# Kernel tuning notes

Measured on AMD Instinct MI355X. Metric: run time of the kernel, lower is better.

## Reference

```python
import jax, jax.numpy as jnp
from jax import lax
import numpy as np

RADIUS = 0.1
NSAMPLE = 32
STRIDE = 3
ED_NSAMPLE = 10


def _sqdist(a, b):
    # a: [B,M,3], b: [B,N,3] -> [B,M,N] squared euclidean distance
    return (jnp.sum(a * a, -1)[:, :, None] + jnp.sum(b * b, -1)[:, None, :]
            - 2.0 * jnp.einsum('bmc,bnc->bmn', a, b))


def setup_inputs() -> dict:
    key = jax.random.key(0)
    ks = jax.random.split(key, 16)
    B, N = 8, 4096
    s = 0.05
    inp = {
        'data': jax.random.normal(ks[0], (B, N, 3), dtype=jnp.float32),
        'numpoints': N,
        # stem MLP 3 -> 64
        'W_stem': jax.random.normal(ks[1], (3, 64), dtype=jnp.float32) * s,
        'b_stem': jnp.zeros((64,), jnp.float32),
        # SA shared MLP (3 dp + 64 fj) -> 128
        'W_sa': jax.random.normal(ks[2], (67, 128), dtype=jnp.float32) * s,
        'b_sa': jnp.zeros((128,), jnp.float32),
        # FP MLP (128 interp + 64 skip) -> 64
        'W_fp': jax.random.normal(ks[3], (192, 64), dtype=jnp.float32) * s,
        'b_fp': jnp.zeros((64,), jnp.float32),
        # eigen-feature MLP 3 -> 4 -> 4
        'W_e1': jax.random.normal(ks[4], (3, 4), dtype=jnp.float32) * s,
        'b_e1': jnp.zeros((4,), jnp.float32),
        'W_e2': jax.random.normal(ks[5], (4, 4), dtype=jnp.float32) * s,
        'b_e2': jnp.zeros((4,), jnp.float32),
        # conv_final 1x1: 68 -> 64, + BN affine
        'W_fin': jax.random.normal(ks[6], (68, 64), dtype=jnp.float32) * s,
        'b_fin': jnp.zeros((64,), jnp.float32),
        'gamma': jnp.ones((64,), jnp.float32),
        'beta': jnp.zeros((64,), jnp.float32),
    }
    return inp


def reference(data, numpoints, W_stem, b_stem, W_sa, b_sa, W_fp, b_fp,
              W_e1, b_e1, W_e2, b_e2, W_fin, b_fin, gamma, beta):
    B, N, _ = data.shape
    b_ix = jnp.arange(B)[:, None, None]

    # ---------- encoder: stem MLP ----------
    f0 = jax.nn.relu(data @ W_stem + b_stem)  # [B,N,64]

    # set abstraction: stride-subsample centers, ball query, dp_fj, MLP, max
    sub_idx = jnp.arange(0, N, STRIDE)
    new_xyz = data[:, sub_idx]                 # [B,M,3]
    d2 = _sqdist(new_xyz, data)                # [B,M,N]
    col = jnp.arange(N, dtype=jnp.int32)
    valid = d2 < RADIUS * RADIUS
    keys = jnp.where(valid, col, N + col)      # first-valid ball query ordering
    negk, _ = lax.top_k(-keys, NSAMPLE)
    idx = -negk                                # [B,M,ns]
    first = idx[..., :1]                       # self point always valid
    idx = jnp.where(idx >= N, first, idx)
    g_xyz = data[b_ix, idx]                    # [B,M,ns,3]
    dp = (g_xyz - new_xyz[:, :, None, :]) / RADIUS  # normalize_dp
    g_f = f0[b_ix, idx]                        # [B,M,ns,64]
    feat = jnp.concatenate([dp, g_f], -1)      # [B,M,ns,67]
    h = jax.nn.relu(feat @ W_sa + b_sa)        # [B,M,ns,128]
    f_sub = jnp.max(h, axis=2)                 # [B,M,128]

    # ---------- decoder: 3-NN inverse-distance feature propagation ----------
    d2f = _sqdist(data, new_xyz)               # [B,N,M]
    negd, nn = lax.top_k(-d2f, 3)
    w = 1.0 / (-negd + 1e-8)
    w = w / jnp.sum(w, -1, keepdims=True)      # [B,N,3]
    nbr_f = f_sub[b_ix, nn]                    # [B,N,3,128]
    interp = jnp.einsum('bnk,bnkc->bnc', w, nbr_f)
    f = jax.nn.relu(jnp.concatenate([interp, f0], -1) @ W_fp + b_fp)  # [B,N,64]

    # ---------- KNN covariance eigen-features ----------
    d2e = _sqdist(data, data)                  # [B,N,N]
    _, gidx = lax.top_k(-d2e, ED_NSAMPLE)      # [B,N,k]
    nbr = data[b_ix, gidx]                     # [B,N,k,3]
    cen = nbr - jnp.mean(nbr, axis=2, keepdims=True)
    cov = jnp.einsum('bnkc,bnkd->bncd', cen, cen) / ED_NSAMPLE  # [B,N,3,3]
    eig = jnp.linalg.eigvalsh(cov)             # [B,N,3] ascending
    ef = jax.nn.relu(eig @ W_e1 + b_e1) @ W_e2 + b_e2  # [B,N,4]

    # ---------- fused 1x1 conv + BN (training-mode stats) + relu ----------
    z_in = jnp.concatenate([f, ef], -1)        # [B,N,68]
    zc = z_in @ W_fin + b_fin                  # [B,N,64]
    mu = jnp.mean(zc, axis=(0, 1))
    var = jnp.var(zc, axis=(0, 1))
    z = jax.nn.relu((zc - mu) * lax.rsqrt(var + 1e-5) * gamma + beta)
    z = jnp.transpose(z, (0, 2, 1))            # [B,64,N]
    return (data, z)
```

## Files before the change

kernel.cpp:

```cpp
#include <hip/hip_runtime.h>
#include <stdint.h>

#define BB 8
#define NN 4096
#define MM 1366
#define NS 32
#define RAD2 0.01f
#define NCH 16
#define CHUNK (NN/NCH)

static_assert(NCH * CHUNK == NN, "chunking");

__device__ __forceinline__ float rl(float v, int l) {
    return __int_as_float(__builtin_amdgcn_readlane(__float_as_int(v), l));
}
__device__ __forceinline__ uint32_t um(uint32_t a, uint32_t b) { return a < b ? a : b; }
__device__ __forceinline__ uint32_t ux(uint32_t a, uint32_t b) { return a > b ? a : b; }
__device__ __forceinline__ uint32_t um3(uint32_t a, uint32_t b, uint32_t c) { return um(um(a, b), c); }

__device__ __forceinline__ void mrg2(uint32_t* kk, uint32_t s0, uint32_t s1) {
    uint32_t n0 = um(kk[0], s0);
    uint32_t n1 = um3(kk[1], ux(kk[0], s0), s1);
    uint32_t n2 = um3(kk[2], ux(kk[1], s0), ux(kk[0], s1));
    uint32_t n3 = um3(kk[3], ux(kk[2], s0), ux(kk[1], s1));
    uint32_t n4 = um3(kk[4], ux(kk[3], s0), ux(kk[2], s1));
    uint32_t n5 = um3(kk[5], ux(kk[4], s0), ux(kk[3], s1));
    uint32_t n6 = um3(kk[6], ux(kk[5], s0), ux(kk[4], s1));
    uint32_t n7 = um3(kk[7], ux(kk[6], s0), ux(kk[5], s1));
    uint32_t n8 = um3(kk[8], ux(kk[7], s0), ux(kk[6], s1));
    uint32_t n9 = um3(kk[9], ux(kk[8], s0), ux(kk[7], s1));
    kk[0]=n0; kk[1]=n1; kk[2]=n2; kk[3]=n3; kk[4]=n4;
    kk[5]=n5; kk[6]=n6; kk[7]=n7; kk[8]=n8; kk[9]=n9;
}

__device__ __forceinline__ void mrg4(uint32_t* kk, uint32_t s0, uint32_t s1,
                                     uint32_t s2, uint32_t s3) {
    uint32_t n0 = um(kk[0], s0);
    uint32_t n1 = um3(kk[1], ux(kk[0], s0), s1);
    uint32_t n2 = um(um3(kk[2], ux(kk[1], s0), ux(kk[0], s1)), s2);
    uint32_t n3 = um3(um3(kk[3], ux(kk[2], s0), ux(kk[1], s1)), ux(kk[0], s2), s3);
    uint32_t n4 = um3(um3(kk[4], ux(kk[3], s0), ux(kk[2], s1)), ux(kk[1], s2), ux(kk[0], s3));
    uint32_t n5 = um3(um3(kk[5], ux(kk[4], s0), ux(kk[3], s1)), ux(kk[2], s2), ux(kk[1], s3));
    uint32_t n6 = um3(um3(kk[6], ux(kk[5], s0), ux(kk[4], s1)), ux(kk[3], s2), ux(kk[2], s3));
    uint32_t n7 = um3(um3(kk[7], ux(kk[6], s0), ux(kk[5], s1)), ux(kk[4], s2), ux(kk[3], s3));
    uint32_t n8 = um3(um3(kk[8], ux(kk[7], s0), ux(kk[6], s1)), ux(kk[5], s2), ux(kk[4], s3));
    uint32_t n9 = um3(um3(kk[9], ux(kk[8], s0), ux(kk[7], s1)), ux(kk[6], s2), ux(kk[5], s3));
    kk[0]=n0; kk[1]=n1; kk[2]=n2; kk[3]=n3; kk[4]=n4;
    kk[5]=n5; kk[6]=n6; kk[7]=n7; kk[8]=n8; kk[9]=n9;
}

__device__ __forceinline__ void srt4(uint32_t& a, uint32_t& b, uint32_t& c, uint32_t& d) {
    uint32_t t0 = um(a, b), t1 = ux(a, b), t2 = um(c, d), t3 = ux(c, d);
    uint32_t s0 = um(t0, t2), m0 = ux(t0, t2), m1 = um(t1, t3), s3 = ux(t1, t3);
    a = s0; b = um(m0, m1); c = ux(m0, m1); d = s3;
}

__global__ __launch_bounds__(256) void k_stem(const float* __restrict__ data,
                                              const float* __restrict__ Ws,
                                              const float* __restrict__ bs,
                                              float* __restrict__ f0,
                                              float* __restrict__ out,
                                              float4* __restrict__ cand4) {
    int blk = blockIdx.x;
    if (blk >= (BB * NN * 64) / 256) {
        int t = (blk - (BB * NN * 64) / 256) * 256 + threadIdx.x;
        float x = data[t * 3], y = data[t * 3 + 1], z = data[t * 3 + 2];
        out[t * 3] = x; out[t * 3 + 1] = y; out[t * 3 + 2] = z;
        cand4[t] = make_float4(x, y, z, x * x + y * y + z * z);
        return;
    }
    int t = blk * 256 + threadIdx.x;
    int c = t & 63;
    int r = t >> 6;
    const float* d = data + r * 3;
    float acc = bs[c];
    acc = fmaf(d[0], Ws[c], acc);
    acc = fmaf(d[1], Ws[64 + c], acc);
    acc = fmaf(d[2], Ws[128 + c], acc);
    f0[t] = fmaxf(acc, 0.f);
}

__global__ __launch_bounds__(256) void k_sa(const float4* __restrict__ cand4,
                                            const float* __restrict__ data,
                                            const float* __restrict__ f0,
                                            const uint32_t* __restrict__ mrg,
                                            const float* __restrict__ Wsa,
                                            const float* __restrict__ bsa,
                                            float* __restrict__ fsub) {
    __shared__ float2 sW[67 * 64];
    __shared__ int sIdx[4][NS];
    for (int i = threadIdx.x; i < 67 * 64; i += 256) {
        int k = i >> 6, c = i & 63;
        sW[i] = make_float2(Wsa[k * 128 + c], Wsa[k * 128 + 64 + c]);
    }
    __syncthreads();
    int wv = threadIdx.x >> 6, lane = threadIdx.x & 63;
    int gm = blockIdx.x * 4 + wv;
    if (gm >= BB * MM) return;
    int b = gm / MM, m = gm - b * MM;
    const float4* cb4 = cand4 + b * NN;
    const float* db = data + b * NN * 3;
    float4 cen = cb4[3 * m];
    float cx = cen.x, cy = cen.y, cz = cen.z, sa = cen.w;

    int cnt;
    bool fallback;
    {
        float d2l = 1e30f;
        int idxl = 0;
        if (lane < 10) {
            uint32_t key = mrg[lane * (BB * NN) + b * NN + 3 * m];
            idxl = (int)(key & 0xFFFu);
            float4 c = cb4[idxl];
            float dot = fmaf(cz, c.z, fmaf(cy, c.y, cx * c.x));
            d2l = (sa + c.w) - 2.f * dot;
        }
        bool valid = (lane < 10) && (d2l < RAD2);
        unsigned long long mask = __ballot(valid);
        if (valid) sIdx[wv][__popcll(mask & ((1ull << lane) - 1ull))] = idxl;
        cnt = __popcll(mask);
        fallback = rl(d2l, 9) < RAD2 * 1.0005f;
    }
    if (fallback) {
        cnt = 0;
        for (int base = 0; base < NN; base += 64) {
            int n = base + lane;
            float4 c = cb4[n];
            float dot = fmaf(cz, c.z, fmaf(cy, c.y, cx * c.x));
            float d2 = (sa + c.w) - 2.f * dot;
            bool valid = d2 < RAD2;
            unsigned long long mask = __ballot(valid);
            if (valid) {
                int pos = cnt + __popcll(mask & ((1ull << lane) - 1ull));
                if (pos < NS) sIdx[wv][pos] = n;
            }
            cnt += __popcll(mask);
            if (cnt >= NS) break;
        }
    }
    int scnt = cnt < NS ? cnt : NS;

    float cl = lane == 0 ? cx : (lane == 1 ? cy : cz);
    float hb0 = bsa[lane], hb1 = bsa[64 + lane];
    float m0 = 0.f, m1 = 0.f;

    for (int s0 = 0; s0 < scnt; s0 += 4) {
        float fr[4], fr2[4];
        #pragma unroll
        for (int u = 0; u < 4; ++u) {
            int s = s0 + u;
            if (s >= scnt) s = 0;
            int nj = sIdx[wv][s];
            int fb = (b * NN + nj) * 64;
            float v;
            if (lane >= 3) v = f0[fb + lane - 3];
            else           v = (db[nj * 3 + lane] - cl) * 10.0f;
            fr[u] = v;
            fr2[u] = (lane < 3) ? f0[fb + 61 + lane] : 0.f;
        }
        float h0[4], h1[4];
        #pragma unroll
        for (int u = 0; u < 4; ++u) { h0[u] = hb0; h1[u] = hb1; }
        for (int k = 0; k < 64; ++k) {
            float2 w = sW[k * 64 + lane];
            #pragma unroll
            for (int u = 0; u < 4; ++u) {
                float fv = rl(fr[u], k);
                h0[u] = fmaf(fv, w.x, h0[u]);
                h1[u] = fmaf(fv, w.y, h1[u]);
            }
        }
        #pragma unroll
        for (int k = 64; k < 67; ++k) {
            float2 w = sW[k * 64 + lane];
            #pragma unroll
            for (int u = 0; u < 4; ++u) {
                float fv = rl(fr2[u], k - 64);
                h0[u] = fmaf(fv, w.x, h0[u]);
                h1[u] = fmaf(fv, w.y, h1[u]);
            }
        }
        #pragma unroll
        for (int u = 0; u < 4; ++u) {
            m0 = fmaxf(m0, fmaxf(h0[u], 0.f));
            m1 = fmaxf(m1, fmaxf(h1[u], 0.f));
        }
    }
    fsub[gm * 128 + lane] = m0;
    fsub[gm * 128 + 64 + lane] = m1;
}

__global__ __launch_bounds__(512) void k_interp(const float4* __restrict__ cand4,
                                                const float* __restrict__ fsub,
                                                float* __restrict__ itp) {
    __shared__ float4 sC[MM];
    __shared__ float sMD[8][64][3];
    __shared__ int   sMI[8][64][3];
    __shared__ float sWts[64][3];
    __shared__ int   sNbr[64][3];
    int t = threadIdx.x, wv = t >> 6, lane = t & 63;
    int blk = blockIdx.x;
    int b = blk >> 6;
    int pbase = (blk & 63) * 64;
    const float4* cb4 = cand4 + b * NN;
    for (int m = t; m < MM; m += 512) sC[m] = cb4[3 * m];
    __syncthreads();
    int p = pbase + lane;
    float4 pm = cb4[p];
    float px = pm.x, py = pm.y, pz = pm.z, pa = pm.w;
    float d0 = 1e30f, d1 = 1e30f, d2v = 1e30f;
    int n0 = 0, n1 = 0, n2 = 0;
    int ms = wv * 171, me = ms + 171 < MM ? ms + 171 : MM;
    for (int m = ms; m < me; ++m) {
        float4 c = sC[m];
        float dd = (pa + c.w) - 2.f * (px * c.x + py * c.y + pz * c.z);
        if (dd < d2v) {
            if (dd < d1) {
                d2v = d1; n2 = n1;
                if (dd < d0) { d1 = d0; n1 = n0; d0 = dd; n0 = m; }
                else         { d1 = dd; n1 = m; }
            } else { d2v = dd; n2 = m; }
        }
    }
    sMD[wv][lane][0] = d0; sMD[wv][lane][1] = d1; sMD[wv][lane][2] = d2v;
    sMI[wv][lane][0] = n0; sMI[wv][lane][1] = n1; sMI[wv][lane][2] = n2;
    __syncthreads();
    if (wv == 0) {
        d0 = sMD[0][lane][0]; d1 = sMD[0][lane][1]; d2v = sMD[0][lane][2];
        n0 = sMI[0][lane][0]; n1 = sMI[0][lane][1]; n2 = sMI[0][lane][2];
        for (int w = 1; w < 8; ++w) {
            #pragma unroll
            for (int r = 0; r < 3; ++r) {
                float dd = sMD[w][lane][r];
                int mm = sMI[w][lane][r];
                if (dd < d2v) {
                    if (dd < d1) {
                        d2v = d1; n2 = n1;
                        if (dd < d0) { d1 = d0; n1 = n0; d0 = dd; n0 = mm; }
                        else         { d1 = dd; n1 = mm; }
                    } else { d2v = dd; n2 = mm; }
                }
            }
        }
        float w0 = 1.f / (d0 + 1e-8f), w1 = 1.f / (d1 + 1e-8f), w2 = 1.f / (d2v + 1e-8f);
        float ws = w0 + w1 + w2;
        sWts[lane][0] = w0 / ws; sWts[lane][1] = w1 / ws; sWts[lane][2] = w2 / ws;
        sNbr[lane][0] = n0; sNbr[lane][1] = n1; sNbr[lane][2] = n2;
    }
    __syncthreads();
    for (int i = wv * 8; i < wv * 8 + 8; ++i) {
        float a0 = sWts[i][0], a1 = sWts[i][1], a2 = sWts[i][2];
        const float* r0 = fsub + (b * MM + sNbr[i][0]) * 128;
        const float* r1 = fsub + (b * MM + sNbr[i][1]) * 128;
        const float* r2 = fsub + (b * MM + sNbr[i][2]) * 128;
        float v0 = fmaf(a2, r2[lane], fmaf(a1, r1[lane], a0 * r0[lane]));
        float v1 = fmaf(a2, r2[64 + lane], fmaf(a1, r1[64 + lane], a0 * r0[64 + lane]));
        int row = b * NN + pbase + i;
        itp[row * 128 + lane] = v0;
        itp[row * 128 + 64 + lane] = v1;
    }
}

__global__ __launch_bounds__(256) void k_knn_part(const float4* __restrict__ cand4,
                                                  uint32_t* __restrict__ pk) {
    int t = threadIdx.x;
    int blk = blockIdx.x;
    int ch = blk & (NCH - 1);
    int pg = (blk >> 4) & 15;
    int b = blk >> 8;
    const float4* cb = cand4 + b * NN;
    int c0 = ch * CHUNK;
    int p = pg * 256 + t;
    float4 me = cb[p];
    float px = me.x, py = me.y, pz = me.z, pa = me.w;
    uint32_t kk[10];
    #pragma unroll
    for (int r = 0; r < 10; ++r) kk[r] = 0xFFFFFF00u + r;
    for (int j = 0; j < CHUNK; j += 4) {
        float4 ca = cb[c0 + j];
        float4 cbv = cb[c0 + j + 1];
        float4 cc = cb[c0 + j + 2];
        float4 cd = cb[c0 + j + 3];
        float da = fmaxf(fmaf(-2.f, fmaf(pz, ca.z, fmaf(py, ca.y, px * ca.x)), pa + ca.w), 0.f);
        float db_ = fmaxf(fmaf(-2.f, fmaf(pz, cbv.z, fmaf(py, cbv.y, px * cbv.x)), pa + cbv.w), 0.f);
        float dc = fmaxf(fmaf(-2.f, fmaf(pz, cc.z, fmaf(py, cc.y, px * cc.x)), pa + cc.w), 0.f);
        float dd = fmaxf(fmaf(-2.f, fmaf(pz, cd.z, fmaf(py, cd.y, px * cd.x)), pa + cd.w), 0.f);
        uint32_t ka = (__float_as_uint(da) & 0xFFFFF000u) | (uint32_t)(c0 + j);
        uint32_t kb = (__float_as_uint(db_) & 0xFFFFF000u) | (uint32_t)(c0 + j + 1);
        uint32_t kc = (__float_as_uint(dc) & 0xFFFFF000u) | (uint32_t)(c0 + j + 2);
        uint32_t kd = (__float_as_uint(dd) & 0xFFFFF000u) | (uint32_t)(c0 + j + 3);
        srt4(ka, kb, kc, kd);
        mrg4(kk, ka, kb, kc, kd);
    }
    int gp = b * NN + p;
    #pragma unroll
    for (int r = 0; r < 10; ++r)
        pk[(ch * 10 + r) * (BB * NN) + gp] = kk[r];
}

__device__ __forceinline__ void jrot(float& app, float& aqq, float& apq,
                                     float& arp, float& arq) {
    float ap = apq;
    if (fabsf(ap) > 1e-32f) {
        float th = (aqq - app) / (2.f * ap);
        float t = 1.f / (fabsf(th) + sqrtf(th * th + 1.f));
        t = th < 0.f ? -t : t;
        float c = 1.f / sqrtf(t * t + 1.f);
        float s = t * c;
        app = app - t * ap;
        aqq = aqq + t * ap;
        apq = 0.f;
        float rp = arp, rq = arq;
        arp = c * rp - s * rq;
        arq = s * rp + c * rq;
    }
}

__global__ __launch_bounds__(256) void k_knn_eig(const float4* __restrict__ cand4,
                                                 const uint32_t* __restrict__ pk,
                                                 uint32_t* __restrict__ mrg,
                                                 const float* __restrict__ We1,
                                                 const float* __restrict__ be1,
                                                 const float* __restrict__ We2,
                                                 const float* __restrict__ be2,
                                                 float* __restrict__ ef) {
    int t = blockIdx.x * 256 + threadIdx.x;
    int b = t >> 12;
    const float4* cb = cand4 + b * NN;
    uint32_t kk[10];
    #pragma unroll
    for (int r = 0; r < 10; ++r) kk[r] = pk[r * (BB * NN) + t];
    for (int ch = 1; ch < NCH; ++ch) {
        uint32_t s[10];
        #pragma unroll
        for (int r = 0; r < 10; ++r) s[r] = pk[(ch * 10 + r) * (BB * NN) + t];
        mrg4(kk, s[0], s[1], s[2], s[3]);
        mrg4(kk, s[4], s[5], s[6], s[7]);
        mrg2(kk, s[8], s[9]);
    }
    #pragma unroll
    for (int r = 0; r < 10; ++r)
        mrg[r * (BB * NN) + t] = kk[r];
    float xs[10], ys[10], zs[10];
    float mx = 0.f, my = 0.f, mz = 0.f;
    #pragma unroll
    for (int r = 0; r < 10; ++r) {
        int n = (int)(kk[r] & 0xFFFu);
        float4 cr = cb[n];
        xs[r] = cr.x; ys[r] = cr.y; zs[r] = cr.z;
        mx += xs[r]; my += ys[r]; mz += zs[r];
    }
    mx *= 0.1f; my *= 0.1f; mz *= 0.1f;
    float a00 = 0, a01 = 0, a02 = 0, a11 = 0, a12 = 0, a22 = 0;
    #pragma unroll
    for (int r = 0; r < 10; ++r) {
        float x = xs[r] - mx, y = ys[r] - my, z = zs[r] - mz;
        a00 = fmaf(x, x, a00); a01 = fmaf(x, y, a01); a02 = fmaf(x, z, a02);
        a11 = fmaf(y, y, a11); a12 = fmaf(y, z, a12); a22 = fmaf(z, z, a22);
    }
    a00 *= 0.1f; a01 *= 0.1f; a02 *= 0.1f; a11 *= 0.1f; a12 *= 0.1f; a22 *= 0.1f;
    #pragma unroll
    for (int sweep = 0; sweep < 6; ++sweep) {
        jrot(a00, a11, a01, a02, a12);
        jrot(a00, a22, a02, a01, a12);
        jrot(a11, a22, a12, a01, a02);
    }
    float e0 = a00, e1 = a11, e2 = a22, tmp;
    if (e0 > e1) { tmp = e0; e0 = e1; e1 = tmp; }
    if (e1 > e2) { tmp = e1; e1 = e2; e2 = tmp; }
    if (e0 > e1) { tmp = e0; e0 = e1; e1 = tmp; }
    float tt[4];
    #pragma unroll
    for (int i = 0; i < 4; ++i) {
        float v = be1[i];
        v = fmaf(e0, We1[i], v);
        v = fmaf(e1, We1[4 + i], v);
        v = fmaf(e2, We1[8 + i], v);
        tt[i] = fmaxf(v, 0.f);
    }
    #pragma unroll
    for (int i = 0; i < 4; ++i) {
        float v = be2[i];
        v = fmaf(tt[0], We2[i], v);
        v = fmaf(tt[1], We2[4 + i], v);
        v = fmaf(tt[2], We2[8 + i], v);
        v = fmaf(tt[3], We2[12 + i], v);
        ef[t * 4 + i] = v;
    }
}

__global__ __launch_bounds__(256) void k_fp(const float* __restrict__ itp,
                                            const float* __restrict__ f0,
                                            const float* __restrict__ W,
                                            const float* __restrict__ bias,
                                            float* __restrict__ outf) {
    __shared__ float sW[192 * 64];
    for (int i = threadIdx.x; i < 192 * 64; i += 256) sW[i] = W[i];
    __syncthreads();
    int lane = threadIdx.x & 63;
    int wv = threadIdx.x >> 6;
    float bb = bias[lane];
    int rowbase = blockIdx.x * 64 + wv * 16;
    for (int it = 0; it < 4; ++it) {
        int r = rowbase + it * 4;
        float fa[4], fbv[4], fc[4], acc[4];
        #pragma unroll
        for (int u = 0; u < 4; ++u) {
            fa[u]  = itp[(r + u) * 128 + lane];
            fbv[u] = itp[(r + u) * 128 + 64 + lane];
            fc[u]  = f0[(r + u) * 64 + lane];
            acc[u] = bb;
        }
        #pragma unroll
        for (int k = 0; k < 192; ++k) {
            float w = sW[k * 64 + lane];
            #pragma unroll
            for (int u = 0; u < 4; ++u) {
                float fv = k < 64 ? rl(fa[u], k)
                         : (k < 128 ? rl(fbv[u], k - 64) : rl(fc[u], k - 128));
                acc[u] = fmaf(fv, w, acc[u]);
            }
        }
        #pragma unroll
        for (int u = 0; u < 4; ++u)
            outf[(r + u) * 64 + lane] = fmaxf(acc[u], 0.f);
    }
}

__global__ __launch_bounds__(256) void k_fin(const float* __restrict__ fb,
                                             const float* __restrict__ efb,
                                             const float* __restrict__ W,
                                             const float* __restrict__ bias,
                                             float* __restrict__ zc) {
    __shared__ float sW[68 * 64];
    for (int i = threadIdx.x; i < 68 * 64; i += 256) sW[i] = W[i];
    __syncthreads();
    int lane = threadIdx.x & 63;
    int wv = threadIdx.x >> 6;
    float bb = bias[lane];
    int rowbase = blockIdx.x * 64 + wv * 16;
    for (int it = 0; it < 4; ++it) {
        int r = rowbase + it * 4;
        float fa[4], fe[4], acc[4];
        #pragma unroll
        for (int u = 0; u < 4; ++u) {
            fa[u] = fb[(r + u) * 64 + lane];
            fe[u] = (lane < 4) ? efb[(r + u) * 4 + lane] : 0.f;
            acc[u] = bb;
        }
        #pragma unroll
        for (int k = 0; k < 68; ++k) {
            float w = sW[k * 64 + lane];
            #pragma unroll
            for (int u = 0; u < 4; ++u) {
                float fv = k < 64 ? rl(fa[u], k) : rl(fe[u], k - 64);
                acc[u] = fmaf(fv, w, acc[u]);
            }
        }
        #pragma unroll
        for (int u = 0; u < 4; ++u)
            zc[(r + u) * 64 + lane] = acc[u];
    }
}

__global__ __launch_bounds__(256) void k_stats1(const float* __restrict__ zc,
                                                float* __restrict__ pp) {
    int t = threadIdx.x;
    int c = t & 63, r4 = t >> 6;
    float s = 0.f, sq = 0.f;
    int base = blockIdx.x * 512;
    for (int i = 0; i < 128; ++i) {
        float v = zc[(base + i * 4 + r4) * 64 + c];
        s += v;
        sq = fmaf(v, v, sq);
    }
    __shared__ float ls[256], lq[256];
    ls[t] = s; lq[t] = sq;
    __syncthreads();
    if (t < 64) {
        float st = ls[t] + ls[t + 64] + ls[t + 128] + ls[t + 192];
        float qt = lq[t] + lq[t + 64] + lq[t + 128] + lq[t + 192];
        pp[blockIdx.x * 128 + t] = st;
        pp[blockIdx.x * 128 + 64 + t] = qt;
    }
}

__global__ __launch_bounds__(64) void k_stats2(const float* __restrict__ pp,
                                               const float* __restrict__ gamma,
                                               const float* __restrict__ beta,
                                               float* __restrict__ ss) {
    int c = threadIdx.x;
    float s = 0.f, sq = 0.f;
    for (int k = 0; k < 64; ++k) {
        s += pp[k * 128 + c];
        sq += pp[k * 128 + 64 + c];
    }
    const float inv = 1.f / (float)(BB * NN);
    float mu = s * inv;
    float var = sq * inv - mu * mu;
    float sc = gamma[c] / sqrtf(var + 1e-5f);
    ss[c] = sc;
    ss[64 + c] = beta[c] - mu * sc;
}

__global__ __launch_bounds__(256) void k_norm_t(const float* __restrict__ zc,
                                                const float* __restrict__ ss,
                                                float* __restrict__ out) {
    __shared__ float sT[64][65];
    int blk = blockIdx.x;
    int b = blk >> 6;
    int nbase = (blk & 63) * 64;
    int c = threadIdx.x & 63;
    int r4 = threadIdx.x >> 6;
    float sc = ss[c], sh = ss[64 + c];
    #pragma unroll
    for (int i = 0; i < 16; ++i) {
        int nr = i * 4 + r4;
        float v = zc[(b * NN + nbase + nr) * 64 + c];
        sT[nr][c] = fmaxf(fmaf(v, sc, sh), 0.f);
    }
    __syncthreads();
    int nn = threadIdx.x & 63;
    #pragma unroll
    for (int i = 0; i < 16; ++i) {
        int cc = i * 4 + r4;
        out[BB * NN * 3 + (b * 64 + cc) * NN + nbase + nn] = sT[nn][cc];
    }
}

extern "C" void kernel_launch(void* const* d_in, const int* in_sizes, int n_in,
                              void* d_out, int out_size, void* d_ws, size_t ws_size,
                              hipStream_t stream) {
    const float* data = (const float*)d_in[0];
    const float* Wst  = (const float*)d_in[2];
    const float* bst  = (const float*)d_in[3];
    const float* Wsa  = (const float*)d_in[4];
    const float* bsa  = (const float*)d_in[5];
    const float* Wfp  = (const float*)d_in[6];
    const float* bfp  = (const float*)d_in[7];
    const float* We1  = (const float*)d_in[8];
    const float* be1  = (const float*)d_in[9];
    const float* We2  = (const float*)d_in[10];
    const float* be2  = (const float*)d_in[11];
    const float* Wfin = (const float*)d_in[12];
    const float* bfin = (const float*)d_in[13];
    const float* gamma = (const float*)d_in[14];
    const float* beta  = (const float*)d_in[15];
    float* out = (float*)d_out;

    float* f0   = (float*)d_ws;
    float* fsub = f0 + 2097152;
    float* efb  = fsub + 1398784;
    float* zc   = efb + 131072;
    float* ss   = zc + 2097152;
    float* pp   = ss + 128;
    float4* cand4 = (float4*)(pp + 8192);
    uint32_t* mrgb = (uint32_t*)((float*)cand4 + 131072);
    float* itp  = (float*)mrgb + 1310720;
    float* fb   = itp + 4194304;
    uint32_t* pkk = (uint32_t*)itp;

    k_stem<<<(BB * NN * 64) / 256 + (BB * NN) / 256, 256, 0, stream>>>(
        data, Wst, bst, f0, out, cand4);
    k_knn_part<<<BB * 16 * NCH, 256, 0, stream>>>(cand4, pkk);
    k_knn_eig<<<(BB * NN) / 256, 256, 0, stream>>>(cand4, pkk, mrgb, We1, be1, We2, be2, efb);
    k_sa<<<(BB * MM + 3) / 4, 256, 0, stream>>>(cand4, data, f0, mrgb, Wsa, bsa, fsub);
    k_interp<<<BB * 64, 512, 0, stream>>>(cand4, fsub, itp);
    k_fp<<<512, 256, 0, stream>>>(itp, f0, Wfp, bfp, fb);
    k_fin<<<512, 256, 0, stream>>>(fb, efb, Wfin, bfin, zc);
    k_stats1<<<64, 256, 0, stream>>>(zc, pp);
    k_stats2<<<1, 64, 0, stream>>>(pp, gamma, beta, ss);
    k_norm_t<<<512, 256, 0, stream>>>(zc, ss, out);
}
```

Baseline: 299.2 us.

## Replace brute-force KNN with Morton-sorted groups and bounding-box pruning

Replaces the brute-force chunked KNN, which compared every point against all 4096 candidates and then merged 16 partial lists, with a spatial approach. A new kernel bins points into a 16^3 Morton grid, counting-sorts them and computes per-group bounding boxes. The new KNN kernel scans its own group first, then visits neighbouring groups in two directions, skipping any whose box distance exceeds the current 10th-nearest bound. The two directional halves are merged in shared memory. This cuts distance work sharply but adds a serial single-block-per-batch sort, a grid of only 512 blocks of 128 threads, and data-dependent divergence.

```diff
diff --git a/kernel.cpp b/kernel.cpp
--- a/kernel.cpp
+++ b/kernel.cpp
@@ -6,10 +6,7 @@
 #define MM 1366
 #define NS 32
 #define RAD2 0.01f
-#define NCH 16
-#define CHUNK (NN/NCH)
-
-static_assert(NCH * CHUNK == NN, "chunking");
+#define NGRP 64
 
 __device__ __forceinline__ float rl(float v, int l) {
     return __int_as_float(__builtin_amdgcn_readlane(__float_as_int(v), l));
@@ -55,6 +52,12 @@
     a = s0; b = um(m0, m1); c = ux(m0, m1); d = s3;
 }
 
+__device__ __forceinline__ uint32_t spr3(uint32_t v) {
+    v = (v | (v << 4)) & 0xC3u;
+    v = (v | (v << 2)) & 0x249u;
+    return v;
+}
+
 __global__ __launch_bounds__(256) void k_stem(const float* __restrict__ data,
                                               const float* __restrict__ Ws,
                                               const float* __restrict__ bs,
@@ -78,6 +81,236 @@
     acc = fmaf(d[1], Ws[64 + c], acc);
     acc = fmaf(d[2], Ws[128 + c], acc);
     f0[t] = fmaxf(acc, 0.f);
+}
+
+__global__ __launch_bounds__(256) void k_sort(const float4* __restrict__ cand4,
+                                              float4* __restrict__ cand4s,
+                                              uint32_t* __restrict__ perm,
+                                              float4* __restrict__ gbox) {
+    __shared__ uint32_t cnt[4096];
+    __shared__ uint32_t part[256];
+    int b = blockIdx.x, t = threadIdx.x;
+    const float4* cb = cand4 + b * NN;
+    for (int i = t; i < 4096; i += 256) cnt[i] = 0;
+    __syncthreads();
+    uint32_t cid[16];
+    #pragma unroll
+    for (int u = 0; u < 16; ++u) {
+        float4 c = cb[u * 256 + t];
+        int ix = (int)floorf((c.x + 4.f) * 2.f);
+        int iy = (int)floorf((c.y + 4.f) * 2.f);
+        int iz = (int)floorf((c.z + 4.f) * 2.f);
+        ix = ix < 0 ? 0 : (ix > 15 ? 15 : ix);
+        iy = iy < 0 ? 0 : (iy > 15 ? 15 : iy);
+        iz = iz < 0 ? 0 : (iz > 15 ? 15 : iz);
+        uint32_t m = spr3((uint32_t)ix) | (spr3((uint32_t)iy) << 1) | (spr3((uint32_t)iz) << 2);
+        cid[u] = m;
+        atomicAdd(&cnt[m], 1u);
+    }
+    __syncthreads();
+    uint32_t c16[16];
+    uint32_t s = 0;
+    #pragma unroll
+    for (int u = 0; u < 16; ++u) { c16[u] = cnt[t * 16 + u]; s += c16[u]; }
+    part[t] = s;
+    __syncthreads();
+    for (int off = 1; off < 256; off <<= 1) {
+        uint32_t v = (t >= off) ? part[t - off] : 0u;
+        __syncthreads();
+        part[t] += v;
+        __syncthreads();
+    }
+    uint32_t run = part[t] - s;
+    #pragma unroll
+    for (int u = 0; u < 16; ++u) { cnt[t * 16 + u] = run; run += c16[u]; }
+    __syncthreads();
+    #pragma unroll
+    for (int u = 0; u < 16; ++u) {
+        int p = u * 256 + t;
+        uint32_t pos = atomicAdd(&cnt[cid[u]], 1u);
+        cand4s[b * NN + pos] = cb[p];
+        perm[b * NN + pos] = (uint32_t)p;
+    }
+    __syncthreads();
+    if (t < NGRP) {
+        float4 mn = make_float4(1e30f, 1e30f, 1e30f, 0.f);
+        float4 mx = make_float4(-1e30f, -1e30f, -1e30f, 0.f);
+        for (int j = 0; j < 64; ++j) {
+            float4 c = cand4s[b * NN + t * 64 + j];
+            mn.x = fminf(mn.x, c.x); mn.y = fminf(mn.y, c.y); mn.z = fminf(mn.z, c.z);
+            mx.x = fmaxf(mx.x, c.x); mx.y = fmaxf(mx.y, c.y); mx.z = fmaxf(mx.z, c.z);
+        }
+        gbox[(b * NGRP + t) * 2]     = mn;
+        gbox[(b * NGRP + t) * 2 + 1] = mx;
+    }
+}
+
+__global__ __launch_bounds__(128) void k_knn(const float4* __restrict__ cand4s,
+                                             const uint32_t* __restrict__ perm,
+                                             const float4* __restrict__ gbox,
+                                             uint32_t* __restrict__ mrg) {
+    __shared__ float4 sBox[2 * NGRP];
+    __shared__ uint32_t sKK[64][10];
+    int t = threadIdx.x, role = t >> 6, lane = t & 63;
+    int gw = blockIdx.x;
+    int b = gw >> 6;
+    int g = gw & (NGRP - 1);
+    for (int i = t; i < 2 * NGRP; i += 128) sBox[i] = gbox[b * 2 * NGRP + i];
+    __syncthreads();
+    const float4* cs = cand4s + b * NN;
+    const uint32_t* ps = perm + b * NN;
+    float4 me = cs[g * 64 + lane];
+    uint32_t mo = ps[g * 64 + lane];
+    float px = me.x, py = me.y, pz = me.z, pa = me.w;
+    uint32_t kk[10];
+    #pragma unroll
+    for (int r = 0; r < 10; ++r) kk[r] = 0xFFFFFF00u + r;
+
+    auto scan_group = [&](int jg) {
+        const float4* cp = cs + jg * 64;
+        const uint4* pq = (const uint4*)(ps + jg * 64);
+        for (int j = 0; j < 16; ++j) {
+            float4 ca  = cp[j * 4];
+            float4 cbv = cp[j * 4 + 1];
+            float4 cc  = cp[j * 4 + 2];
+            float4 cd  = cp[j * 4 + 3];
+            uint4 pm = pq[j];
+            float da  = fmaxf(fmaf(-2.f, fmaf(pz, ca.z,  fmaf(py, ca.y,  px * ca.x)),  pa + ca.w),  0.f);
+            float db_ = fmaxf(fmaf(-2.f, fmaf(pz, cbv.z, fmaf(py, cbv.y, px * cbv.x)), pa + cbv.w), 0.f);
+            float dc  = fmaxf(fmaf(-2.f, fmaf(pz, cc.z,  fmaf(py, cc.y,  px * cc.x)),  pa + cc.w),  0.f);
+            float dd  = fmaxf(fmaf(-2.f, fmaf(pz, cd.z,  fmaf(py, cd.y,  px * cd.x)),  pa + cd.w),  0.f);
+            uint32_t ka = (__float_as_uint(da)  & 0xFFFFF000u) | pm.x;
+            uint32_t kb = (__float_as_uint(db_) & 0xFFFFF000u) | pm.y;
+            uint32_t kc = (__float_as_uint(dc)  & 0xFFFFF000u) | pm.z;
+            uint32_t kd = (__float_as_uint(dd)  & 0xFFFFF000u) | pm.w;
+            uint32_t mn4 = um(um(ka, kb), um(kc, kd));
+            if (__ballot(mn4 < kk[9])) {
+                srt4(ka, kb, kc, kd);
+                mrg4(kk, ka, kb, kc, kd);
+            }
+        }
+    };
+    auto bound = [&]() {
+        float u2 = __uint_as_float((kk[9] & 0xFFFFF000u) + 0x1000u);
+        #pragma unroll
+        for (int off = 1; off < 64; off <<= 1) u2 = fmaxf(u2, __shfl_xor(u2, off));
+        return u2;
+    };
+
+    scan_group(g);
+    float ub = bound();
+    float4 amn = sBox[g * 2], amx = sBox[g * 2 + 1];
+    auto try_group = [&](int jg) {
+        float4 bmn = sBox[jg * 2], bmx = sBox[jg * 2 + 1];
+        float dx = fmaxf(fmaxf(amn.x - bmx.x, bmn.x - amx.x), 0.f);
+        float dy = fmaxf(fmaxf(amn.y - bmx.y, bmn.y - amx.y), 0.f);
+        float dz = fmaxf(fmaxf(amn.z - bmx.z, bmn.z - amx.z), 0.f);
+        float bd2 = fmaf(dx, dx, fmaf(dy, dy, dz * dz));
+        if (bd2 < ub * 1.0005f) {
+            scan_group(jg);
+            ub = bound();
+        }
+    };
+    if (role == 0) {
+        for (int d = 1; d < NGRP; ++d) { int j = g - d; if (j >= 0)   try_group(j); }
+    } else {
+        for (int d = 1; d < NGRP; ++d) { int j = g + d; if (j < NGRP) try_group(j); }
+    }
+    if (role == 1) {
+        #pragma unroll
+        for (int r = 0; r < 10; ++r) sKK[lane][r] = kk[r];
+    }
+    __syncthreads();
+    if (role == 0) {
+        uint32_t s[10];
+        #pragma unroll
+        for (int r = 0; r < 10; ++r) s[r] = sKK[lane][r];
+        mrg4(kk, s[0], s[1], s[2], s[3]);
+        mrg4(kk, s[4], s[5], s[6], s[7]);
+        mrg2(kk, s[8], s[9]);
+        int gp = b * NN + (int)mo;
+        #pragma unroll
+        for (int r = 0; r < 10; ++r) mrg[r * (BB * NN) + gp] = kk[r];
+    }
+}
+
+__device__ __forceinline__ void jrot(float& app, float& aqq, float& apq,
+                                     float& arp, float& arq) {
+    float ap = apq;
+    if (fabsf(ap) > 1e-32f) {
+        float th = (aqq - app) / (2.f * ap);
+        float t = 1.f / (fabsf(th) + sqrtf(th * th + 1.f));
+        t = th < 0.f ? -t : t;
+        float c = 1.f / sqrtf(t * t + 1.f);
+        float s = t * c;
+        app = app - t * ap;
+        aqq = aqq + t * ap;
+        apq = 0.f;
+        float rp = arp, rq = arq;
+        arp = c * rp - s * rq;
+        arq = s * rp + c * rq;
+    }
+}
+
+__global__ __launch_bounds__(256) void k_knn_eig(const float4* __restrict__ cand4,
+                                                 const uint32_t* __restrict__ mrg,
+                                                 const float* __restrict__ We1,
+                                                 const float* __restrict__ be1,
+                                                 const float* __restrict__ We2,
+                                                 const float* __restrict__ be2,
+                                                 float* __restrict__ ef) {
+    int t = blockIdx.x * 256 + threadIdx.x;
+    int b = t >> 12;
+    const float4* cb = cand4 + b * NN;
+    uint32_t kk[10];
+    #pragma unroll
+    for (int r = 0; r < 10; ++r) kk[r] = mrg[r * (BB * NN) + t];
+    float xs[10], ys[10], zs[10];
+    float mx = 0.f, my = 0.f, mz = 0.f;
+    #pragma unroll
+    for (int r = 0; r < 10; ++r) {
+        int n = (int)(kk[r] & 0xFFFu);
+        float4 cr = cb[n];
+        xs[r] = cr.x; ys[r] = cr.y; zs[r] = cr.z;
+        mx += xs[r]; my += ys[r]; mz += zs[r];
+    }
+    mx *= 0.1f; my *= 0.1f; mz *= 0.1f;
+    float a00 = 0, a01 = 0, a02 = 0, a11 = 0, a12 = 0, a22 = 0;
+    #pragma unroll
+    for (int r = 0; r < 10; ++r) {
+        float x = xs[r] - mx, y = ys[r] - my, z = zs[r] - mz;
+        a00 = fmaf(x, x, a00); a01 = fmaf(x, y, a01); a02 = fmaf(x, z, a02);
+        a11 = fmaf(y, y, a11); a12 = fmaf(y, z, a12); a22 = fmaf(z, z, a22);
+    }
+    a00 *= 0.1f; a01 *= 0.1f; a02 *= 0.1f; a11 *= 0.1f; a12 *= 0.1f; a22 *= 0.1f;
+    #pragma unroll
+    for (int sweep = 0; sweep < 6; ++sweep) {
+        jrot(a00, a11, a01, a02, a12);
+        jrot(a00, a22, a02, a01, a12);
+        jrot(a11, a22, a12, a01, a02);
+    }
+    float e0 = a00, e1 = a11, e2 = a22, tmp;
+    if (e0 > e1) { tmp = e0; e0 = e1; e1 = tmp; }
+    if (e1 > e2) { tmp = e1; e1 = e2; e2 = tmp; }
+    if (e0 > e1) { tmp = e0; e0 = e1; e1 = tmp; }
+    float tt[4];
+    #pragma unroll
+    for (int i = 0; i < 4; ++i) {
+        float v = be1[i];
+        v = fmaf(e0, We1[i], v);
+        v = fmaf(e1, We1[4 + i], v);
+        v = fmaf(e2, We1[8 + i], v);
+        tt[i] = fmaxf(v, 0.f);
+    }
+    #pragma unroll
+    for (int i = 0; i < 4; ++i) {
+        float v = be2[i];
+        v = fmaf(tt[0], We2[i], v);
+        v = fmaf(tt[1], We2[4 + i], v);
+        v = fmaf(tt[2], We2[8 + i], v);
+        v = fmaf(tt[3], We2[12 + i], v);
+        ef[t * 4 + i] = v;
+    }
 }
 
 __global__ __launch_bounds__(256) void k_sa(const float4* __restrict__ cand4,
@@ -258,134 +491,6 @@
         int row = b * NN + pbase + i;
         itp[row * 128 + lane] = v0;
         itp[row * 128 + 64 + lane] = v1;
-    }
-}
-
-__global__ __launch_bounds__(256) void k_knn_part(const float4* __restrict__ cand4,
-                                                  uint32_t* __restrict__ pk) {
-    int t = threadIdx.x;
-    int blk = blockIdx.x;
-    int ch = blk & (NCH - 1);
-    int pg = (blk >> 4) & 15;
-    int b = blk >> 8;
-    const float4* cb = cand4 + b * NN;
-    int c0 = ch * CHUNK;
-    int p = pg * 256 + t;
-    float4 me = cb[p];
-    float px = me.x, py = me.y, pz = me.z, pa = me.w;
-    uint32_t kk[10];
-    #pragma unroll
-    for (int r = 0; r < 10; ++r) kk[r] = 0xFFFFFF00u + r;
-    for (int j = 0; j < CHUNK; j += 4) {
-        float4 ca = cb[c0 + j];
-        float4 cbv = cb[c0 + j + 1];
-        float4 cc = cb[c0 + j + 2];
-        float4 cd = cb[c0 + j + 3];
-        float da = fmaxf(fmaf(-2.f, fmaf(pz, ca.z, fmaf(py, ca.y, px * ca.x)), pa + ca.w), 0.f);
-        float db_ = fmaxf(fmaf(-2.f, fmaf(pz, cbv.z, fmaf(py, cbv.y, px * cbv.x)), pa + cbv.w), 0.f);
-        float dc = fmaxf(fmaf(-2.f, fmaf(pz, cc.z, fmaf(py, cc.y, px * cc.x)), pa + cc.w), 0.f);
-        float dd = fmaxf(fmaf(-2.f, fmaf(pz, cd.z, fmaf(py, cd.y, px * cd.x)), pa + cd.w), 0.f);
-        uint32_t ka = (__float_as_uint(da) & 0xFFFFF000u) | (uint32_t)(c0 + j);
-        uint32_t kb = (__float_as_uint(db_) & 0xFFFFF000u) | (uint32_t)(c0 + j + 1);
-        uint32_t kc = (__float_as_uint(dc) & 0xFFFFF000u) | (uint32_t)(c0 + j + 2);
-        uint32_t kd = (__float_as_uint(dd) & 0xFFFFF000u) | (uint32_t)(c0 + j + 3);
-        srt4(ka, kb, kc, kd);
-        mrg4(kk, ka, kb, kc, kd);
-    }
-    int gp = b * NN + p;
-    #pragma unroll
-    for (int r = 0; r < 10; ++r)
-        pk[(ch * 10 + r) * (BB * NN) + gp] = kk[r];
-}
-
-__device__ __forceinline__ void jrot(float& app, float& aqq, float& apq,
-                                     float& arp, float& arq) {
-    float ap = apq;
-    if (fabsf(ap) > 1e-32f) {
-        float th = (aqq - app) / (2.f * ap);
-        float t = 1.f / (fabsf(th) + sqrtf(th * th + 1.f));
-        t = th < 0.f ? -t : t;
-        float c = 1.f / sqrtf(t * t + 1.f);
-        float s = t * c;
-        app = app - t * ap;
-        aqq = aqq + t * ap;
-        apq = 0.f;
-        float rp = arp, rq = arq;
-        arp = c * rp - s * rq;
-        arq = s * rp + c * rq;
-    }
-}
-
-__global__ __launch_bounds__(256) void k_knn_eig(const float4* __restrict__ cand4,
-                                                 const uint32_t* __restrict__ pk,
-                                                 uint32_t* __restrict__ mrg,
-                                                 const float* __restrict__ We1,
-                                                 const float* __restrict__ be1,
-                                                 const float* __restrict__ We2,
-                                                 const float* __restrict__ be2,
-                                                 float* __restrict__ ef) {
-    int t = blockIdx.x * 256 + threadIdx.x;
-    int b = t >> 12;
-    const float4* cb = cand4 + b * NN;
-    uint32_t kk[10];
-    #pragma unroll
-    for (int r = 0; r < 10; ++r) kk[r] = pk[r * (BB * NN) + t];
-    for (int ch = 1; ch < NCH; ++ch) {
-        uint32_t s[10];
-        #pragma unroll
-        for (int r = 0; r < 10; ++r) s[r] = pk[(ch * 10 + r) * (BB * NN) + t];
-        mrg4(kk, s[0], s[1], s[2], s[3]);
-        mrg4(kk, s[4], s[5], s[6], s[7]);
-        mrg2(kk, s[8], s[9]);
-    }
-    #pragma unroll
-    for (int r = 0; r < 10; ++r)
-        mrg[r * (BB * NN) + t] = kk[r];
-    float xs[10], ys[10], zs[10];
-    float mx = 0.f, my = 0.f, mz = 0.f;
-    #pragma unroll
-    for (int r = 0; r < 10; ++r) {
-        int n = (int)(kk[r] & 0xFFFu);
-        float4 cr = cb[n];
-        xs[r] = cr.x; ys[r] = cr.y; zs[r] = cr.z;
-        mx += xs[r]; my += ys[r]; mz += zs[r];
-    }
-    mx *= 0.1f; my *= 0.1f; mz *= 0.1f;
-    float a00 = 0, a01 = 0, a02 = 0, a11 = 0, a12 = 0, a22 = 0;
-    #pragma unroll
-    for (int r = 0; r < 10; ++r) {
-        float x = xs[r] - mx, y = ys[r] - my, z = zs[r] - mz;
-        a00 = fmaf(x, x, a00); a01 = fmaf(x, y, a01); a02 = fmaf(x, z, a02);
-        a11 = fmaf(y, y, a11); a12 = fmaf(y, z, a12); a22 = fmaf(z, z, a22);
-    }
-    a00 *= 0.1f; a01 *= 0.1f; a02 *= 0.1f; a11 *= 0.1f; a12 *= 0.1f; a22 *= 0.1f;
-    #pragma unroll
-    for (int sweep = 0; sweep < 6; ++sweep) {
-        jrot(a00, a11, a01, a02, a12);
-        jrot(a00, a22, a02, a01, a12);
-        jrot(a11, a22, a12, a01, a02);
-    }
-    float e0 = a00, e1 = a11, e2 = a22, tmp;
-    if (e0 > e1) { tmp = e0; e0 = e1; e1 = tmp; }
-    if (e1 > e2) { tmp = e1; e1 = e2; e2 = tmp; }
-    if (e0 > e1) { tmp = e0; e0 = e1; e1 = tmp; }
-    float tt[4];
-    #pragma unroll
-    for (int i = 0; i < 4; ++i) {
-        float v = be1[i];
-        v = fmaf(e0, We1[i], v);
-        v = fmaf(e1, We1[4 + i], v);
-        v = fmaf(e2, We1[8 + i], v);
-        tt[i] = fmaxf(v, 0.f);
-    }
-    #pragma unroll
-    for (int i = 0; i < 4; ++i) {
-        float v = be2[i];
-        v = fmaf(tt[0], We2[i], v);
-        v = fmaf(tt[1], We2[4 + i], v);
-        v = fmaf(tt[2], We2[8 + i], v);
-        v = fmaf(tt[3], We2[12 + i], v);
-        ef[t * 4 + i] = v;
     }
 }
 
@@ -558,12 +663,15 @@
     uint32_t* mrgb = (uint32_t*)((float*)cand4 + 131072);
     float* itp  = (float*)mrgb + 1310720;
     float* fb   = itp + 4194304;
-    uint32_t* pkk = (uint32_t*)itp;
+    float4*   cand4s = (float4*)itp;
+    uint32_t* perm   = (uint32_t*)(itp + 131072);
+    float4*   gbox   = (float4*)(itp + 131072 + 32768);
 
     k_stem<<<(BB * NN * 64) / 256 + (BB * NN) / 256, 256, 0, stream>>>(
         data, Wst, bst, f0, out, cand4);
-    k_knn_part<<<BB * 16 * NCH, 256, 0, stream>>>(cand4, pkk);
-    k_knn_eig<<<(BB * NN) / 256, 256, 0, stream>>>(cand4, pkk, mrgb, We1, be1, We2, be2, efb);
+    k_sort<<<BB, 256, 0, stream>>>(cand4, cand4s, perm, gbox);
+    k_knn<<<BB * NGRP, 128, 0, stream>>>(cand4s, perm, gbox, mrgb);
+    k_knn_eig<<<(BB * NN) / 256, 256, 0, stream>>>(cand4, mrgb, We1, be1, We2, be2, efb);
     k_sa<<<(BB * MM + 3) / 4, 256, 0, stream>>>(cand4, data, f0, mrgb, Wsa, bsa, fsub);
     k_interp<<<BB * 64, 512, 0, stream>>>(cand4, fsub, itp);
     k_fp<<<512, 256, 0, stream>>>(itp, f0, Wfp, bfp, fb);
```

New measurement: 474.0 us. 58.4% more time.
